# Optimization experiments

Measured on AMD Instinct MI355X. Metric: run time of the kernel, lower is better.

Reference implementation:

```python
import jax, jax.numpy as jnp
import numpy as np

B, S, D = 2, 2048, 2048
H, G = 16, 4
DH = D // H  # 128
KV = G * DH  # 512


def setup_inputs() -> dict:
    key = jax.random.key(0)
    ks = jax.random.split(key, 10)
    scale = 1.0 / np.sqrt(D)
    hidden_state = jax.random.normal(ks[0], (B, S, D), dtype=jnp.float32)
    # causal mask: 1 above the diagonal (positions to block), 0 elsewhere
    casual_mask = jnp.triu(jnp.ones((S, S), dtype=jnp.float32), k=1)
    padding_mask = jnp.zeros((B, S), dtype=jnp.float32)
    Wq = jax.random.normal(ks[1], (D, D), dtype=jnp.float32) * scale
    bq = jnp.zeros((D,), dtype=jnp.float32)
    Wk = jax.random.normal(ks[2], (D, KV), dtype=jnp.float32) * scale
    bk = jnp.zeros((KV,), dtype=jnp.float32)
    Wv = jax.random.normal(ks[3], (D, KV), dtype=jnp.float32) * scale
    bv = jnp.zeros((KV,), dtype=jnp.float32)
    Wo = jax.random.normal(ks[4], (D, D), dtype=jnp.float32) * scale
    bo = jnp.zeros((D,), dtype=jnp.float32)
    return {"hidden_state": hidden_state, "casual_mask": casual_mask,
            "padding_mask": padding_mask, "Wq": Wq, "bq": bq, "Wk": Wk,
            "bk": bk, "Wv": Wv, "bv": bv, "Wo": Wo, "bo": bo}


def reference(hidden_state, casual_mask, padding_mask, Wq, bq, Wk, bk, Wv, bv, Wo, bo):
    b, s, _ = hidden_state.shape
    rep = H // G  # heads per KV group
    q = (hidden_state @ Wq + bq).reshape(b, s, H, DH).transpose(0, 2, 1, 3)  # [b,H,s,dh]
    k = (hidden_state @ Wk + bk).reshape(b, s, G, DH).transpose(0, 2, 1, 3)  # [b,G,s,dh]
    v = (hidden_state @ Wv + bv).reshape(b, s, G, DH).transpose(0, 2, 1, 3)
    # expand KV heads: each group serves H//G query heads
    k = jnp.repeat(k, rep, axis=1)  # [b,H,s,dh]
    v = jnp.repeat(v, rep, axis=1)
    scores = jnp.einsum('bhqd,bhkd->bhqk', q, k) / jnp.sqrt(jnp.float32(DH))
    scores = scores + casual_mask * (-1e9)
    scores = scores + padding_mask[:, None, None, :] * (-1e9)
    attn = jax.nn.softmax(scores, axis=-1)
    out = jnp.einsum('bhqk,bhkd->bhqd', attn, v)  # [b,H,s,dh]
    out = out.transpose(0, 2, 1, 3).reshape(b, s, D)
    return out @ Wo + bo
```

## Files before the change

### kernel.cpp

```cpp
#include <hip/hip_runtime.h>
#include <math.h>

typedef unsigned short u16;
typedef __bf16 bf16_t;
typedef u16 u16x4 __attribute__((ext_vector_type(4)));
typedef u16 u16x8 __attribute__((ext_vector_type(8)));
typedef bf16_t bf16x8 __attribute__((ext_vector_type(8)));
typedef float f32x4 __attribute__((ext_vector_type(4)));

__device__ __forceinline__ float bf2f(u16 v) {
    union { unsigned u; float f; } x; x.u = ((unsigned)v) << 16; return x.f;
}
__device__ __forceinline__ u16 f2bf(float f) {
    union { float f; unsigned u; } x; x.f = f;
    unsigned u = x.u;
    return (u16)((u + 0x7fffu + ((u >> 16) & 1u)) >> 16);
}

__device__ __forceinline__ void gload16(const u16* g, u16* l) {
    __builtin_amdgcn_global_load_lds(
        (const __attribute__((address_space(1))) void*)g,
        (__attribute__((address_space(3))) void*)l,
        16, 0, 0);
}

#define POWS_UNITS 436

__device__ __forceinline__ bool is_bf16_input(const unsigned* __restrict__ probe) {
    unsigned w = probe[(threadIdx.x & 63) * 32771 + 7];
    unsigned b7 = (w >> 8) & 0x7f;
    bool hit = (b7 >= 0x38) && (b7 <= 0x3f);
    return __builtin_popcountll(__ballot(hit)) >= 32;
}

__global__ __launch_bounds__(256) void convert_kernel(
    const void* __restrict__ src, u16* __restrict__ dst, int n,
    const unsigned* __restrict__ probe)
{
    bool bf = is_bf16_input(probe);
    int i = (blockIdx.x * 256 + threadIdx.x) * 8;
    if (i >= n) return;
    if (bf) {
        *(u16x8*)&dst[i] = *(const u16x8*)&((const u16*)src)[i];
    } else {
        const float* s = (const float*)src + i;
        u16x8 o;
#pragma unroll
        for (int j = 0; j < 8; j++) o[j] = f2bf(s[j]);
        *(u16x8*)&dst[i] = o;
    }
}

__global__ __launch_bounds__(256) void tconv_kernel(
    const void* __restrict__ in, u16* __restrict__ out, int R, int C,
    const unsigned* __restrict__ probe)
{
    bool bf = is_bf16_input(probe);
    __shared__ u16 t[32][33];
    int x = threadIdx.x & 31, y = threadIdx.x >> 5;
    int bx = blockIdx.x * 32, by = blockIdx.y * 32;
    if (bf) {
        const u16* s = (const u16*)in;
#pragma unroll
        for (int i = 0; i < 32; i += 8)
            t[y + i][x] = s[(size_t)(by + y + i) * C + bx + x];
    } else {
        const float* s = (const float*)in;
#pragma unroll
        for (int i = 0; i < 32; i += 8)
            t[y + i][x] = f2bf(s[(size_t)(by + y + i) * C + bx + x]);
    }
    __syncthreads();
#pragma unroll
    for (int i = 0; i < 32; i += 8)
        out[(size_t)(bx + y + i) * R + by + x] = t[x][y + i];
}

__global__ __launch_bounds__(256) void transpose_kernel(
    const u16* __restrict__ in, u16* __restrict__ out, int R, int LD)
{
    __shared__ u16 t[32][33];
    int x = threadIdx.x & 31, y = threadIdx.x >> 5;
    int bx = blockIdx.x * 32, by = blockIdx.y * 32;
#pragma unroll
    for (int i = 0; i < 32; i += 8)
        t[y + i][x] = in[(size_t)(by + y + i) * LD + bx + x];
    __syncthreads();
#pragma unroll
    for (int i = 0; i < 32; i += 8)
        out[(size_t)(bx + y + i) * R + by + x] = t[x][y + i];
}

__global__ __launch_bounds__(256) void gemm_bias_kernel(
    const u16* __restrict__ A, const u16* __restrict__ BT,
    const void* __restrict__ bias0, const void* __restrict__ bias1,
    const void* __restrict__ bias2, void* __restrict__ Cout,
    int M, int N, int K, const unsigned* __restrict__ probe,
    int out_native, float scale)
{
    __shared__ __align__(16) u16 As[128 * 32];
    __shared__ __align__(16) u16 Bs[128 * 32];
    const int tid  = threadIdx.x;
    const int lane = tid & 63, wave = tid >> 6;
    const int quad = lane >> 4, li = lane & 15;
    const int bm = blockIdx.x * 128, bn = blockIdx.y * 128;
    const int wm = (wave >> 1) * 64, wn = (wave & 1) * 64;
    const int lrow = lane >> 2;
    const int lcol = (lane & 3) * 8;

    f32x4 acc[4][4] = {};

    for (int k0 = 0; k0 < K; k0 += 32) {
#pragma unroll
        for (int j = 0; j < 2; j++) {
            int c = wave * 2 + j;
            int row = c * 16 + lrow;
            gload16(&A [(size_t)(bm + row) * K + k0 + lcol], &As[c * 16 * 32]);
            gload16(&BT[(size_t)(bn + row) * K + k0 + lcol], &Bs[c * 16 * 32]);
        }
        __syncthreads();
        bf16x8 af[4], bfr[4];
#pragma unroll
        for (int i = 0; i < 4; i++)
            af[i]  = *(const bf16x8*)&As[(wm + i * 16 + li) * 32 + quad * 8];
#pragma unroll
        for (int i = 0; i < 4; i++)
            bfr[i] = *(const bf16x8*)&Bs[(wn + i * 16 + li) * 32 + quad * 8];
#pragma unroll
        for (int mt = 0; mt < 4; mt++)
#pragma unroll
            for (int nt = 0; nt < 4; nt++)
                acc[mt][nt] = __builtin_amdgcn_mfma_f32_16x16x32_bf16(
                    af[mt], bfr[nt], acc[mt][nt], 0, 0, 0);
        __syncthreads();
    }

    const bool bf_in = is_bf16_input(probe);
    const bool out_bf = out_native ? bf_in : true;
#pragma unroll
    for (int nt = 0; nt < 4; nt++) {
        int col = bn + wn + nt * 16 + li;
        const void* bp; int bc;
        if (col < 2048)      { bp = bias0; bc = col; }
        else if (col < 2560) { bp = bias1; bc = col - 2048; }
        else                 { bp = bias2; bc = col - 2560; }
        float bb = bf_in ? bf2f(((const u16*)bp)[bc]) : ((const float*)bp)[bc];
        if (out_bf) {
            u16* C16 = (u16*)Cout;
#pragma unroll
            for (int mt = 0; mt < 4; mt++)
#pragma unroll
                for (int r = 0; r < 4; r++) {
                    int row = bm + wm + mt * 16 + quad * 4 + r;
                    C16[(size_t)row * N + col] = f2bf((acc[mt][nt][r] + bb) * scale);
                }
        } else {
            float* Cf = (float*)Cout;
#pragma unroll
            for (int mt = 0; mt < 4; mt++)
#pragma unroll
                for (int r = 0; r < 4; r++) {
                    int row = bm + wm + mt * 16 + quad * 4 + r;
                    Cf[(size_t)row * N + col] = (acc[mt][nt][r] + bb) * scale;
                }
        }
    }
}

__global__ __launch_bounds__(256) void flash_kernel(
    const u16* __restrict__ Q, const u16* __restrict__ Kg,
    const u16* __restrict__ VT, u16* __restrict__ O,
    float* __restrict__ POws, float* __restrict__ POdout,
    float* __restrict__ PM, float* __restrict__ PL)
{
    constexpr int S = 2048, D = 2048, DH = 128, QKSTR = 3072;
    constexpr float SCALE = 0.08838834764831845f;
    __shared__ __align__(16) u16 Ks[32 * 136];
    __shared__ __align__(16) u16 Vt[128 * 40];
    __shared__ __align__(16) u16 Pw[4][32 * 40];

    const int tid  = threadIdx.x;
    const int wave = tid >> 6, lane = tid & 63;
    const int quad = lane >> 4, li = lane & 15;
    const int uu = blockIdx.x, h = blockIdx.y, b = blockIdx.z;
    int qt, cc, nc;
    if (uu < 7)       { qt = uu;                         cc = 0;          nc = 1; }
    else if (uu < 21) { int t = uu - 7;  qt = 7 + (t >> 1);  cc = t & 1;  nc = 2; }
    else              { int t = uu - 21; qt = 14 + t / 3;    cc = t % 3;  nc = 3; }
    const int T = qt + 1;
    const int tb = T / nc, trem = T % nc;
    const int tcnt = tb + (cc < trem ? 1 : 0);
    const int tstart = cc * tb + (cc < trem ? cc : trem);
    const int kstart = tstart * 128;
    const int kend   = (tstart + tcnt) * 128;
    const int g = h >> 2;
    const int q0w = qt * 128 + wave * 32;

    const u16* Qb = Q  + (size_t)b * S * QKSTR;
    const u16* Kb = Kg + (size_t)b * S * QKSTR;
    const u16* Vg = VT + (size_t)g * DH * (2 * S) + (size_t)b * S;

    bf16x8 qf[2][4];
#pragma unroll
    for (int m = 0; m < 2; m++)
#pragma unroll
        for (int c = 0; c < 4; c++)
            qf[m][c] = *(const bf16x8*)&Qb[(size_t)(q0w + m * 16 + li) * QKSTR
                                           + h * DH + c * 32 + quad * 8];

    f32x4 oacc[2][8] = {};
    float mr[2] = { -INFINITY, -INFINITY };
    float lr[2] = { 0.f, 0.f };

    u16x8 kreg[2], vreg[2];
#pragma unroll
    for (int ch = 0; ch < 2; ch++) {
        int idx = tid + ch * 256;
        kreg[ch] = *(const u16x8*)&Kb[(size_t)(kstart + (idx >> 4)) * QKSTR
                                      + g * DH + (idx & 15) * 8];
        vreg[ch] = *(const u16x8*)&Vg[(size_t)(idx >> 2) * (2 * S)
                                      + kstart + (idx & 3) * 8];
    }

    for (int kc = kstart; kc < kend; kc += 32) {
#pragma unroll
        for (int ch = 0; ch < 2; ch++) {
            int idx = tid + ch * 256;
            *(u16x8*)&Ks[(idx >> 4) * 136 + (idx & 15) * 8] = kreg[ch];
            *(u16x8*)&Vt[(idx >> 2) * 40  + (idx & 3) * 8]  = vreg[ch];
        }
        __syncthreads();

        int kn = kc + 32;
        if (kn < kend) {
#pragma unroll
            for (int ch = 0; ch < 2; ch++) {
                int idx = tid + ch * 256;
                kreg[ch] = *(const u16x8*)&Kb[(size_t)(kn + (idx >> 4)) * QKSTR
                                              + g * DH + (idx & 15) * 8];
                vreg[ch] = *(const u16x8*)&Vg[(size_t)(idx >> 2) * (2 * S)
                                              + kn + (idx & 3) * 8];
            }
        }

        if (kc <= q0w) {
            f32x4 sacc[2][2] = {};
#pragma unroll
            for (int t = 0; t < 2; t++)
#pragma unroll
                for (int c = 0; c < 4; c++) {
                    bf16x8 kf = *(const bf16x8*)&Ks[(t * 16 + li) * 136 + c * 32 + quad * 8];
#pragma unroll
                    for (int m = 0; m < 2; m++)
                        sacc[m][t] = __builtin_amdgcn_mfma_f32_16x16x32_bf16(
                            kf, qf[m][c], sacc[m][t], 0, 0, 0);
                }

            float alpha_b[2][4];
#pragma unroll
            for (int m = 0; m < 2; m++) {
                int row = q0w + m * 16 + li;
                f32x4 s0 = sacc[m][0] * SCALE;
                f32x4 s1 = sacc[m][1] * SCALE;
#pragma unroll
                for (int r = 0; r < 4; r++) {
                    int k0 = kc + quad * 4 + r;
                    if (k0 > row)      s0[r] = -INFINITY;
                    if (k0 + 16 > row) s1[r] = -INFINITY;
                }
                float mx = fmaxf(fmaxf(fmaxf(s0[0], s0[1]), fmaxf(s0[2], s0[3])),
                                 fmaxf(fmaxf(s1[0], s1[1]), fmaxf(s1[2], s1[3])));
                mx = fmaxf(mx, __shfl_xor(mx, 16));
                mx = fmaxf(mx, __shfl_xor(mx, 32));
                float mnew = fmaxf(mr[m], mx);
                float al = __expf(mr[m] - mnew);
                mr[m] = mnew;
                f32x4 p0, p1;
                float ps = 0.f;
#pragma unroll
                for (int r = 0; r < 4; r++) {
                    p0[r] = __expf(s0[r] - mnew);
                    p1[r] = __expf(s1[r] - mnew);
                    ps += p0[r] + p1[r];
                }
                ps += __shfl_xor(ps, 16);
                ps += __shfl_xor(ps, 32);
                lr[m] = lr[m] * al + ps;
                u16x4 c0, c1;
#pragma unroll
                for (int r = 0; r < 4; r++) { c0[r] = f2bf(p0[r]); c1[r] = f2bf(p1[r]); }
                *(u16x4*)&Pw[wave][(m * 16 + li) * 40 + quad * 4]      = c0;
                *(u16x4*)&Pw[wave][(m * 16 + li) * 40 + 16 + quad * 4] = c1;
#pragma unroll
                for (int r = 0; r < 4; r++)
                    alpha_b[m][r] = __shfl(al, quad * 4 + r, 16);
            }

#pragma unroll
            for (int m = 0; m < 2; m++)
#pragma unroll
                for (int dt = 0; dt < 8; dt++)
#pragma unroll
                    for (int r = 0; r < 4; r++)
                        oacc[m][dt][r] *= alpha_b[m][r];

            asm volatile("s_waitcnt lgkmcnt(0)" ::: "memory");
            union { u16x8 u; bf16x8 bv; } pc0, pc1;
            pc0.u = *(const u16x8*)&Pw[wave][(0 * 16 + li) * 40 + quad * 8];
            pc1.u = *(const u16x8*)&Pw[wave][(1 * 16 + li) * 40 + quad * 8];
            bf16x8 pf[2] = { pc0.bv, pc1.bv };

#pragma unroll
            for (int dt = 0; dt < 8; dt++) {
                bf16x8 vf = *(const bf16x8*)&Vt[(dt * 16 + li) * 40 + quad * 8];
#pragma unroll
                for (int m = 0; m < 2; m++)
                    oacc[m][dt] = __builtin_amdgcn_mfma_f32_16x16x32_bf16(
                        pf[m], vf, oacc[m][dt], 0, 0, 0);
            }
        }
        __syncthreads();
    }

    if (nc == 1) {
        u16* Ob = O + (size_t)b * S * D;
#pragma unroll
        for (int m = 0; m < 2; m++) {
#pragma unroll
            for (int r = 0; r < 4; r++) {
                float linv = 1.0f / __shfl(lr[m], quad * 4 + r, 16);
                int row = q0w + m * 16 + quad * 4 + r;
#pragma unroll
                for (int dt = 0; dt < 8; dt++)
                    Ob[(size_t)row * D + h * DH + dt * 16 + li] =
                        f2bf(oacc[m][dt][r] * linv);
            }
        }
    } else {
        const int pl = (qt <= 13) ? (qt - 7) * 2 + cc : 14 + (qt - 14) * 3 + cc;
        const int pg = (b * 16 + h) * 20 + pl;
        float* POu = (pg < POWS_UNITS)
                   ? (POws   + (size_t)pg * 16384)
                   : (POdout + (size_t)(pg - POWS_UNITS) * 16384);
#pragma unroll
        for (int m = 0; m < 2; m++)
#pragma unroll
            for (int r = 0; r < 4; r++) {
                int rl = wave * 32 + m * 16 + quad * 4 + r;
#pragma unroll
                for (int dt = 0; dt < 8; dt++)
                    POu[rl * 128 + dt * 16 + li] = oacc[m][dt][r];
            }
        if (quad == 0) {
#pragma unroll
            for (int m = 0; m < 2; m++) {
                int rl = wave * 32 + m * 16 + li;
                PM[pg * 128 + rl] = mr[m];
                PL[pg * 128 + rl] = lr[m];
            }
        }
    }
}

__global__ __launch_bounds__(256) void combine_kernel(
    const float* __restrict__ POws, const float* __restrict__ POdout,
    const float* __restrict__ PM, const float* __restrict__ PL,
    u16* __restrict__ O)
{
    constexpr int S = 2048, D = 2048;
    const int qt = 7 + blockIdx.x, h = blockIdx.y, b = blockIdx.z;
    const int nc = (qt <= 13) ? 2 : 3;
    const int pl0 = (qt <= 13) ? (qt - 7) * 2 : 14 + (qt - 14) * 3;
    const int pg0 = (b * 16 + h) * 20 + pl0;
    const int t = threadIdx.x;
    const int row = t >> 1, half = (t & 1) * 64;

    float m[3], l[3], w[3];
    const float* p[3];
    float M = -INFINITY;
    for (int i = 0; i < nc; i++) {
        int pg = pg0 + i;
        m[i] = PM[pg * 128 + row];
        l[i] = PL[pg * 128 + row];
        M = fmaxf(M, m[i]);
        p[i] = ((pg < POWS_UNITS)
                ? (POws   + (size_t)pg * 16384)
                : (POdout + (size_t)(pg - POWS_UNITS) * 16384))
               + row * 128 + half;
    }
    float lsum = 0.f;
    for (int i = 0; i < nc; i++) { w[i] = __expf(m[i] - M); lsum += w[i] * l[i]; }
    float linv = 1.0f / lsum;

    u16* out = O + (size_t)(b * S + qt * 128 + row) * D + h * 128 + half;
#pragma unroll 4
    for (int j = 0; j < 64; j += 4) {
        f32x4 acc = {};
        for (int i = 0; i < nc; i++) {
            f32x4 a = *(const f32x4*)&p[i][j];
#pragma unroll
            for (int e = 0; e < 4; e++) acc[e] += a[e] * w[i];
        }
        u16x4 o;
#pragma unroll
        for (int e = 0; e < 4; e++) o[e] = f2bf(acc[e] * linv);
        *(u16x4*)&out[j] = o;
    }
}

extern "C" void kernel_launch(void* const* d_in, const int* in_sizes, int n_in,
                              void* d_out, int out_size, void* d_ws, size_t ws_size,
                              hipStream_t stream)
{
    const void* X  = d_in[0];
    const void* Wq = d_in[3];
    const void* bq = d_in[4];
    const void* Wk = d_in[5];
    const void* bk = d_in[6];
    const void* Wv = d_in[7];
    const void* bv = d_in[8];
    const void* Wo = d_in[9];
    const void* bo = d_in[10];
    const unsigned* probe = (const unsigned*)d_in[3];

    u16* ws    = (u16*)d_ws;
    u16* Xc    = ws;
    u16* WqkvT = Xc    + 8388608;
    u16* QKV   = WqkvT + 6291456;
    u16* VTb   = QKV   + 12582912;
    u16* Ob    = VTb   + 2097152;
    float* POws   = (float*)ws;
    float* PM     = POws + (size_t)POWS_UNITS * 16384;
    float* PL     = PM + 640 * 128;
    float* POdout = (float*)d_out;

    convert_kernel<<<4096, 256, 0, stream>>>(X, Xc, 8388608, probe);

    tconv_kernel<<<dim3(64, 64), 256, 0, stream>>>(Wq, WqkvT,               2048, 2048, probe);
    tconv_kernel<<<dim3(16, 64), 256, 0, stream>>>(Wk, WqkvT + 2048 * 2048, 2048, 512,  probe);
    tconv_kernel<<<dim3(16, 64), 256, 0, stream>>>(Wv, WqkvT + 2560 * 2048, 2048, 512,  probe);

    gemm_bias_kernel<<<dim3(32, 24), 256, 0, stream>>>(
        Xc, WqkvT, bq, bk, bv, QKV, 4096, 3072, 2048, probe, 0, 1.0f);

    transpose_kernel<<<dim3(16, 128), 256, 0, stream>>>(QKV + 2560, VTb, 4096, 3072);

    flash_kernel<<<dim3(27, 16, 2), 256, 0, stream>>>(
        QKV, QKV + 2048, VTb, Ob, POws, POdout, PM, PL);

    combine_kernel<<<dim3(9, 16, 2), 256, 0, stream>>>(POws, POdout, PM, PL, Ob);

    tconv_kernel<<<dim3(64, 64), 256, 0, stream>>>(Wo, WqkvT, 2048, 2048, probe);

    gemm_bias_kernel<<<dim3(32, 16), 256, 0, stream>>>(
        Ob, WqkvT, bo, bo, bo, d_out, 4096, 2048, 2048, probe, 1, 1.0f);
}
```

Before: 427.8 us.

## Fuse input conversion kernels and read V fragments directly from global

Merges the X conversion and the three weight transpose-convert launches into one prep kernel that picks its job from the block index, removing three kernel launches. In the flash kernel, V is no longer staged through shared memory; each wave loads its V^T MFMA fragments straight from global memory. This cuts LDS traffic and register prefetch, but adds uncoalesced, unprefetched global loads in the inner loop that every wave repeats.

```diff
diff --git a/kernel.cpp b/kernel.cpp
--- a/kernel.cpp
+++ b/kernel.cpp
@@ -33,22 +33,57 @@
     return __builtin_popcountll(__ballot(hit)) >= 32;
 }
 
-__global__ __launch_bounds__(256) void convert_kernel(
-    const void* __restrict__ src, u16* __restrict__ dst, int n,
+__global__ __launch_bounds__(256) void prep_kernel(
+    const void* __restrict__ X, u16* __restrict__ Xc,
+    const void* __restrict__ Wq, const void* __restrict__ Wk,
+    const void* __restrict__ Wv, u16* __restrict__ WqkvT,
     const unsigned* __restrict__ probe)
 {
-    bool bf = is_bf16_input(probe);
-    int i = (blockIdx.x * 256 + threadIdx.x) * 8;
-    if (i >= n) return;
+    __shared__ u16 t[32][33];
+    const bool bf = is_bf16_input(probe);
+    const int bid = blockIdx.x;
+
+    if (bid < 4096) {
+        int i = (bid * 256 + threadIdx.x) * 8;
+        if (bf) {
+            *(u16x8*)&Xc[i] = *(const u16x8*)&((const u16*)X)[i];
+        } else {
+            const float* s = (const float*)X + i;
+            u16x8 o;
+#pragma unroll
+            for (int j = 0; j < 8; j++) o[j] = f2bf(s[j]);
+            *(u16x8*)&Xc[i] = o;
+        }
+        return;
+    }
+
+    const void* in; u16* out; int R, C, bx, by;
+    if (bid < 8192) {
+        int b2 = bid - 4096; in = Wq; out = WqkvT;
+        R = 2048; C = 2048; bx = (b2 & 63) * 32; by = (b2 >> 6) * 32;
+    } else if (bid < 9216) {
+        int b2 = bid - 8192; in = Wk; out = WqkvT + 2048 * 2048;
+        R = 2048; C = 512; bx = (b2 & 15) * 32; by = (b2 >> 4) * 32;
+    } else {
+        int b2 = bid - 9216; in = Wv; out = WqkvT + 2560 * 2048;
+        R = 2048; C = 512; bx = (b2 & 15) * 32; by = (b2 >> 4) * 32;
+    }
+    int x = threadIdx.x & 31, y = threadIdx.x >> 5;
     if (bf) {
-        *(u16x8*)&dst[i] = *(const u16x8*)&((const u16*)src)[i];
+        const u16* s = (const u16*)in;
+#pragma unroll
+        for (int i = 0; i < 32; i += 8)
+            t[y + i][x] = s[(size_t)(by + y + i) * C + bx + x];
     } else {
-        const float* s = (const float*)src + i;
-        u16x8 o;
-#pragma unroll
-        for (int j = 0; j < 8; j++) o[j] = f2bf(s[j]);
-        *(u16x8*)&dst[i] = o;
-    }
+        const float* s = (const float*)in;
+#pragma unroll
+        for (int i = 0; i < 32; i += 8)
+            t[y + i][x] = f2bf(s[(size_t)(by + y + i) * C + bx + x]);
+    }
+    __syncthreads();
+#pragma unroll
+    for (int i = 0; i < 32; i += 8)
+        out[(size_t)(bx + y + i) * R + by + x] = t[x][y + i];
 }
 
 __global__ __launch_bounds__(256) void tconv_kernel(
@@ -176,7 +211,6 @@
     constexpr int S = 2048, D = 2048, DH = 128, QKSTR = 3072;
     constexpr float SCALE = 0.08838834764831845f;
     __shared__ __align__(16) u16 Ks[32 * 136];
-    __shared__ __align__(16) u16 Vt[128 * 40];
     __shared__ __align__(16) u16 Pw[4][32 * 40];
 
     const int tid  = threadIdx.x;
@@ -212,14 +246,12 @@
     float mr[2] = { -INFINITY, -INFINITY };
     float lr[2] = { 0.f, 0.f };
 
-    u16x8 kreg[2], vreg[2];
+    u16x8 kreg[2];
 #pragma unroll
     for (int ch = 0; ch < 2; ch++) {
         int idx = tid + ch * 256;
         kreg[ch] = *(const u16x8*)&Kb[(size_t)(kstart + (idx >> 4)) * QKSTR
                                       + g * DH + (idx & 15) * 8];
-        vreg[ch] = *(const u16x8*)&Vg[(size_t)(idx >> 2) * (2 * S)
-                                      + kstart + (idx & 3) * 8];
     }
 
     for (int kc = kstart; kc < kend; kc += 32) {
@@ -227,7 +259,6 @@
         for (int ch = 0; ch < 2; ch++) {
             int idx = tid + ch * 256;
             *(u16x8*)&Ks[(idx >> 4) * 136 + (idx & 15) * 8] = kreg[ch];
-            *(u16x8*)&Vt[(idx >> 2) * 40  + (idx & 3) * 8]  = vreg[ch];
         }
         __syncthreads();
 
@@ -238,8 +269,6 @@
                 int idx = tid + ch * 256;
                 kreg[ch] = *(const u16x8*)&Kb[(size_t)(kn + (idx >> 4)) * QKSTR
                                               + g * DH + (idx & 15) * 8];
-                vreg[ch] = *(const u16x8*)&Vg[(size_t)(idx >> 2) * (2 * S)
-                                              + kn + (idx & 3) * 8];
             }
         }
 
@@ -312,7 +341,8 @@
 
 #pragma unroll
             for (int dt = 0; dt < 8; dt++) {
-                bf16x8 vf = *(const bf16x8*)&Vt[(dt * 16 + li) * 40 + quad * 8];
+                bf16x8 vf = *(const bf16x8*)&Vg[(size_t)(dt * 16 + li) * (2 * S)
+                                                + kc + quad * 8];
 #pragma unroll
                 for (int m = 0; m < 2; m++)
                     oacc[m][dt] = __builtin_amdgcn_mfma_f32_16x16x32_bf16(
@@ -434,11 +464,7 @@
     float* PL     = PM + 640 * 128;
     float* POdout = (float*)d_out;
 
-    convert_kernel<<<4096, 256, 0, stream>>>(X, Xc, 8388608, probe);
-
-    tconv_kernel<<<dim3(64, 64), 256, 0, stream>>>(Wq, WqkvT,               2048, 2048, probe);
-    tconv_kernel<<<dim3(16, 64), 256, 0, stream>>>(Wk, WqkvT + 2048 * 2048, 2048, 512,  probe);
-    tconv_kernel<<<dim3(16, 64), 256, 0, stream>>>(Wv, WqkvT + 2560 * 2048, 2048, 512,  probe);
+    prep_kernel<<<10240, 256, 0, stream>>>(X, Xc, Wq, Wk, Wv, WqkvT, probe);
 
     gemm_bias_kernel<<<dim3(32, 24), 256, 0, stream>>>(
         Xc, WqkvT, bq, bk, bv, QKV, 4096, 3072, 2048, probe, 0, 1.0f);
```

Result: no change. 433.0 us (+1.2%).
